# Optimization experiments

Hardware: AMD Instinct MI355X
Metric: run time of the kernel (lower is better)

## Reference

```python
import jax, jax.numpy as jnp
import numpy as np
import math

N_NODES = 50000
N_EDGES = 800000
F_IN = 32
HID = 64


def _layernorm(x, g, b, eps=1e-5):
    mu = x.mean(-1, keepdims=True)
    var = ((x - mu) ** 2).mean(-1, keepdims=True)
    return (x - mu) / jnp.sqrt(var + eps) * g + b


def _tconv(x, src, dst, Wq, bq, Wk, bk, Wv, bv, Ws, heads):
    # PyG TransformerConv (concat=True, root_weight=True, bias=False on skip)
    N = x.shape[0]
    C = Wq.shape[1] // heads
    q = (x @ Wq + bq).reshape(N, heads, C)[dst]  # [E,H,C] gathered at targets
    k = (x @ Wk + bk).reshape(N, heads, C)[src]  # [E,H,C] gathered at sources
    v = (x @ Wv + bv).reshape(N, heads, C)[src]
    scores = (q * k).sum(-1) / math.sqrt(C)      # [E,H]
    m = jax.ops.segment_max(scores, dst, num_segments=N)   # [N,H]
    p = jnp.exp(scores - m[dst])
    denom = jax.ops.segment_sum(p, dst, num_segments=N)
    alpha = p / (denom[dst] + 1e-16)             # segment softmax over in-edges
    agg = jax.ops.segment_sum(v * alpha[..., None], dst, num_segments=N)
    return agg.reshape(N, heads * C) + x @ Ws    # + skip (no bias)


def setup_inputs() -> dict:
    key = jax.random.key(0)
    ks = iter(jax.random.split(key, 64))
    def rn(shape, s=0.1):
        return jax.random.normal(next(ks), shape, jnp.float32) * s
    inp = {
        "x": rn((N_NODES, F_IN), 1.0),
        "edge_index": jax.random.randint(next(ks), (2, N_EDGES), 0, N_NODES, dtype=jnp.int32),
        "ln0_g": jnp.ones((F_IN,), jnp.float32),
        "ln0_b": jnp.zeros((F_IN,), jnp.float32),
    }
    dims = [F_IN, HID, HID]
    for l in range(3):
        d = dims[l]
        inp[f"Wq{l}"] = rn((d, HID)); inp[f"bq{l}"] = rn((HID,), 0.05)
        inp[f"Wk{l}"] = rn((d, HID)); inp[f"bk{l}"] = rn((HID,), 0.05)
        inp[f"Wv{l}"] = rn((d, HID)); inp[f"bv{l}"] = rn((HID,), 0.05)
        inp[f"Ws{l}"] = rn((d, HID))
        inp[f"g{l}"] = jnp.ones((HID,), jnp.float32)
        inp[f"b{l}"] = jnp.zeros((HID,), jnp.float32)
    inp["Wr1"] = rn((HID, HID // 2)); inp["br1"] = jnp.zeros((HID // 2,), jnp.float32)
    inp["Wr2"] = rn((HID // 2, 1));   inp["br2"] = jnp.zeros((1,), jnp.float32)
    inp["Wt1"] = rn((HID, HID // 2)); inp["bt1"] = jnp.zeros((HID // 2,), jnp.float32)
    inp["Wt2"] = rn((HID // 2, 1));   inp["bt2"] = jnp.zeros((1,), jnp.float32)
    return inp


def reference(x, edge_index, ln0_g, ln0_b,
              Wq0, bq0, Wk0, bk0, Wv0, bv0, Ws0, g0, b0,
              Wq1, bq1, Wk1, bk1, Wv1, bv1, Ws1, g1, b1,
              Wq2, bq2, Wk2, bk2, Wv2, bv2, Ws2, g2, b2,
              Wr1, br1, Wr2, br2, Wt1, bt1, Wt2, bt2):
    src, dst = edge_index[0], edge_index[1]
    h = _layernorm(x, ln0_g, ln0_b)
    layers = [
        (Wq0, bq0, Wk0, bk0, Wv0, bv0, Ws0, g0, b0, 4),
        (Wq1, bq1, Wk1, bk1, Wv1, bv1, Ws1, g1, b1, 4),
        (Wq2, bq2, Wk2, bk2, Wv2, bv2, Ws2, g2, b2, 1),
    ]
    for i, (Wq, bq, Wk, bk, Wv, bv, Ws, g, b, heads) in enumerate(layers):
        x_res = h if h.shape[-1] == HID else None
        h = _tconv(h, src, dst, Wq, bq, Wk, bk, Wv, bv, Ws, heads)
        h = _layernorm(h, g, b)
        if x_res is not None and i > 0:
            h = h + 0.1 * x_res
        if i < len(layers) - 1:
            h = jax.nn.relu(h)  # dropout is identity in eval mode
    rtt = jax.nn.relu(h @ Wr1 + br1) @ Wr2 + br2      # [N,1]
    retrans = jax.nn.relu(h @ Wt1 + bt1) @ Wt2 + bt2  # [N,1]
    return jnp.concatenate([rtt, retrans], axis=1)    # [N,2]
```

## Files before the change

### kernel.cpp

```cpp
#include <hip/hip_runtime.h>
#include <hip/hip_bf16.h>
#include <math.h>

#define N_NODES 50000
#define N_EDGES 800000
#define HID 64
#define NBK 196
#define EPB 1024
#define SB  ((N_EDGES + EPB - 1) / EPB)
#define FLAT (NBK * SB)
#define SCAN_B ((FLAT + 255) / 256)

#define LN0_BLKS   6250
#define HIST_BLKS  SB
#define WP0_BLKS   32
#define WP12_BLKS  64
#define PREP_BLKS  (LN0_BLKS + HIST_BLKS + WP0_BLKS + 2 * WP12_BLKS)

typedef __attribute__((ext_vector_type(8))) short short8;
typedef __attribute__((ext_vector_type(4))) float float4v;

__device__ __forceinline__ unsigned short f32_to_bf16_rne(float f) {
    unsigned int u = __float_as_uint(f);
    unsigned int r = u + 0x7fffu + ((u >> 16) & 1u);
    return (unsigned short)(r >> 16);
}

__device__ __forceinline__ void ln0_body(int b, int t,
        const float* __restrict__ x, const float* __restrict__ g,
        const float* __restrict__ bb, float* __restrict__ h0) {
    int lane = t & 63;
    int n = b * 8 + (t >> 6) * 2 + (lane >> 5);
    int c = lane & 31;
    float v = x[n * 32 + c];
    float s = v;
    #pragma unroll
    for (int off = 1; off < 32; off <<= 1) s += __shfl_xor(s, off);
    float mu = s * (1.0f / 32.0f);
    float d = v - mu;
    float vs = d * d;
    #pragma unroll
    for (int off = 1; off < 32; off <<= 1) vs += __shfl_xor(vs, off);
    float var = vs * (1.0f / 32.0f);
    h0[n * 32 + c] = d * rsqrtf(var + 1e-5f) * g[c] + bb[c];
}

__device__ __forceinline__ void wprep_body(int idx, int KS,
        const float* __restrict__ Wq, const float* __restrict__ Wk,
        const float* __restrict__ Wv, const float* __restrict__ Ws,
        unsigned short* __restrict__ Wp) {
    int j = idx & 7;
    int lane = (idx >> 3) & 63;
    int ts = idx >> 9;
    int s = ts % KS;
    int tile = ts / KS;
    int which = tile >> 2;
    int slice = tile & 3;
    int k = s * 32 + ((lane >> 4) * 8) + j;
    int col = slice * 16 + (lane & 15);
    const float* W = (which == 0) ? Wq : (which == 1) ? Wk : (which == 2) ? Wv : Ws;
    Wp[idx] = f32_to_bf16_rne(W[k * 64 + col]);
}

__global__ __launch_bounds__(256) void prep_kernel(
        const float* __restrict__ x, const float* __restrict__ ln0g,
        const float* __restrict__ ln0b, float* __restrict__ h0,
        const int* __restrict__ dst, int* __restrict__ ghist,
        const float* __restrict__ Wq0, const float* __restrict__ Wk0,
        const float* __restrict__ Wv0, const float* __restrict__ Ws0,
        unsigned short* __restrict__ Wp0,
        const float* __restrict__ Wq1, const float* __restrict__ Wk1,
        const float* __restrict__ Wv1, const float* __restrict__ Ws1,
        unsigned short* __restrict__ Wp1,
        const float* __restrict__ Wq2, const float* __restrict__ Wk2,
        const float* __restrict__ Wv2, const float* __restrict__ Ws2,
        unsigned short* __restrict__ Wp2) {
    __shared__ int hist[NBK];
    int b = blockIdx.x;
    int t = threadIdx.x;
    if (b < LN0_BLKS) {
        ln0_body(b, t, x, ln0g, ln0b, h0);
    } else if (b < LN0_BLKS + HIST_BLKS) {
        int i = b - LN0_BLKS;
        for (int k = t; k < NBK; k += 256) hist[k] = 0;
        __syncthreads();
        int e0 = i * EPB;
        #pragma unroll
        for (int r = 0; r < EPB / 256; r++) {
            int e = e0 + r * 256 + t;
            if (e < N_EDGES) atomicAdd(&hist[dst[e] >> 8], 1);
        }
        __syncthreads();
        for (int k = t; k < NBK; k += 256) ghist[k * SB + i] = hist[k];
    } else if (b < LN0_BLKS + HIST_BLKS + WP0_BLKS) {
        int idx = (b - LN0_BLKS - HIST_BLKS) * 256 + t;
        wprep_body(idx, 1, Wq0, Wk0, Wv0, Ws0, Wp0);
    } else if (b < LN0_BLKS + HIST_BLKS + WP0_BLKS + WP12_BLKS) {
        int idx = (b - LN0_BLKS - HIST_BLKS - WP0_BLKS) * 256 + t;
        wprep_body(idx, 2, Wq1, Wk1, Wv1, Ws1, Wp1);
    } else {
        int idx = (b - LN0_BLKS - HIST_BLKS - WP0_BLKS - WP12_BLKS) * 256 + t;
        wprep_body(idx, 2, Wq2, Wk2, Wv2, Ws2, Wp2);
    }
}

__global__ void scan1_kernel(const int* __restrict__ ghist, int* __restrict__ csum) {
    int f = blockIdx.x * 256 + threadIdx.x;
    int v = (f < FLAT) ? ghist[f] : 0;
    #pragma unroll
    for (int off = 1; off < 64; off <<= 1) v += __shfl_xor(v, off);
    __shared__ int ws[4];
    if ((threadIdx.x & 63) == 0) ws[threadIdx.x >> 6] = v;
    __syncthreads();
    if (threadIdx.x == 0) csum[blockIdx.x] = ws[0] + ws[1] + ws[2] + ws[3];
}

__global__ void scan2_kernel(const int* __restrict__ csum, int* __restrict__ coff,
                             int* __restrict__ bbase, int* __restrict__ row_ptr) {
    int lane = threadIdx.x;
    int carry = 0;
    for (int base = 0; base < SCAN_B; base += 64) {
        int i = base + lane;
        int v = (i < SCAN_B) ? csum[i] : 0;
        int incl = v;
        #pragma unroll
        for (int off = 1; off < 64; off <<= 1) {
            int tt = __shfl_up(incl, off);
            if (lane >= off) incl += tt;
        }
        if (i < SCAN_B) coff[i] = carry + incl - v;
        carry += __shfl(incl, 63);
    }
    if (lane == 0) { bbase[NBK] = N_EDGES; row_ptr[N_NODES] = N_EDGES; }
}

__global__ void scan3_kernel(const int* __restrict__ ghist, const int* __restrict__ coff,
                             int* __restrict__ goff, int* __restrict__ bbase) {
    int f = blockIdx.x * 256 + threadIdx.x;
    int lane = threadIdx.x & 63;
    int w = threadIdx.x >> 6;
    int v = (f < FLAT) ? ghist[f] : 0;
    int incl = v;
    #pragma unroll
    for (int off = 1; off < 64; off <<= 1) {
        int tt = __shfl_up(incl, off);
        if (lane >= off) incl += tt;
    }
    __shared__ int ws[4];
    if (lane == 63) ws[w] = incl;
    __syncthreads();
    int woff = 0;
    #pragma unroll
    for (int k = 0; k < 4; k++) if (k < w) woff += ws[k];
    int excl = coff[blockIdx.x] + woff + incl - v;
    if (f < FLAT) {
        goff[f] = excl;
        if (f % SB == 0) bbase[f / SB] = excl;
    }
}

__global__ __launch_bounds__(256) void scatter_kernel(
        const int* __restrict__ src, const int* __restrict__ dst,
        const int* __restrict__ goff, int2* __restrict__ ebkt) {
    __shared__ int hist[NBK];
    int t = threadIdx.x, i = blockIdx.x;
    for (int k = t; k < NBK; k += 256) hist[k] = 0;
    __syncthreads();
    int e0 = i * EPB;
    #pragma unroll
    for (int r = 0; r < EPB / 256; r++) {
        int e = e0 + r * 256 + t;
        if (e < N_EDGES) {
            int s = src[e], d = dst[e];
            int k = d >> 8;
            int rank = atomicAdd(&hist[k], 1);
            ebkt[goff[k * SB + i] + rank] = make_int2(s, d);
        }
    }
}

__global__ __launch_bounds__(256) void bucket_build_kernel(
        const int2* __restrict__ ebkt, const int* __restrict__ bbase,
        int* __restrict__ row_ptr, int* __restrict__ colb) {
    __shared__ int ldeg[256];
    __shared__ int lcur[256];
    __shared__ int wsum[4];
    int b = blockIdx.x;
    int t = threadIdx.x;
    int cbase = bbase[b];
    int cnt = bbase[b + 1] - cbase;

    ldeg[t] = 0;
    __syncthreads();
    for (int i = t; i < cnt; i += 256) {
        int2 e = ebkt[cbase + i];
        atomicAdd(&ldeg[e.y & 255], 1);
    }
    __syncthreads();

    int lane = t & 63;
    int w = t >> 6;
    int v = ldeg[t];
    int incl = v;
    #pragma unroll
    for (int off = 1; off < 64; off <<= 1) {
        int tt = __shfl_up(incl, off);
        if (lane >= off) incl += tt;
    }
    if (lane == 63) wsum[w] = incl;
    __syncthreads();
    int woff = 0;
    #pragma unroll
    for (int k = 0; k < 4; k++) if (k < w) woff += wsum[k];
    int excl = woff + incl - v;

    int node = b * 256 + t;
    if (node < N_NODES) row_ptr[node] = cbase + excl;
    lcur[t] = excl;
    __syncthreads();

    for (int i = t; i < cnt; i += 256) {
        int2 e = ebkt[cbase + i];
        int r = atomicAdd(&lcur[e.y & 255], 1);
        colb[cbase + r] = e.x;
    }
}

template <int D>
__global__ __launch_bounds__(256) void qkvs_mfma_kernel(
        const float* __restrict__ h,
        const unsigned short* __restrict__ Wp,
        const float* __restrict__ bq, const float* __restrict__ bk,
        const float* __restrict__ bv,
        float* __restrict__ Q, unsigned int* __restrict__ KV,
        float* __restrict__ S) {
    constexpr int KS = D / 32;
    int t = threadIdx.x;
    int lane = t & 63;
    int w = t >> 6;
    int n0 = blockIdx.x * 16;
    int n16 = lane & 15;
    int quad = lane >> 4;
    int col = w * 16 + n16;

    short8 afrag[KS];
    #pragma unroll
    for (int s = 0; s < KS; s++) {
        const float* hp = &h[(n0 + n16) * D + s * 32 + quad * 8];
        float4 a0 = *(const float4*)hp;
        float4 a1 = *(const float4*)(hp + 4);
        short8 af;
        af[0] = (short)f32_to_bf16_rne(a0.x);
        af[1] = (short)f32_to_bf16_rne(a0.y);
        af[2] = (short)f32_to_bf16_rne(a0.z);
        af[3] = (short)f32_to_bf16_rne(a0.w);
        af[4] = (short)f32_to_bf16_rne(a1.x);
        af[5] = (short)f32_to_bf16_rne(a1.y);
        af[6] = (short)f32_to_bf16_rne(a1.z);
        af[7] = (short)f32_to_bf16_rne(a1.w);
        afrag[s] = af;
    }

    float4v accs[4];
    #pragma unroll
    for (int which = 0; which < 4; which++) {
        float4v acc = {0.0f, 0.0f, 0.0f, 0.0f};
        int tile = which * 4 + w;
        #pragma unroll
        for (int s = 0; s < KS; s++) {
            short8 bfrag = *(const short8*)&Wp[((tile * KS + s) * 64 + lane) * 8];
            acc = __builtin_amdgcn_mfma_f32_16x16x32_bf16(afrag[s], bfrag, acc, 0, 0, 0);
        }
        accs[which] = acc;
    }

    float bqc = bq[col], bkc = bk[col], bvc = bv[col];

    #pragma unroll
    for (int r = 0; r < 4; r++) {
        int node = n0 + quad * 4 + r;
        Q[node * 64 + col] = accs[0][r] + bqc;
        unsigned int kw = f32_to_bf16_rne(accs[1][r] + bkc);
        unsigned int vw = f32_to_bf16_rne(accs[2][r] + bvc);
        KV[node * 64 + col] = (vw << 16) | kw;
        S[node * 64 + col] = accs[3][r];
    }
}

template <int HEADS, bool RES, bool RELU, bool HEAD>
__global__ __launch_bounds__(256) void agg_kernel(
                           const float* __restrict__ Q, const unsigned int* __restrict__ KV,
                           const float* __restrict__ S,
                           const int* __restrict__ row_ptr, const int* __restrict__ colb,
                           const float* __restrict__ g, const float* __restrict__ b,
                           const float* __restrict__ h_in, float* __restrict__ h_out,
                           const float* __restrict__ Wr1, const float* __restrict__ br1,
                           const float* __restrict__ Wr2, const float* __restrict__ br2,
                           const float* __restrict__ Wt1, const float* __restrict__ bt1,
                           const float* __restrict__ Wt2, const float* __restrict__ bt2,
                           float* __restrict__ out) {
    constexpr int C = HID / HEADS;
    int lane = threadIdx.x & 63;
    int m = lane & 15;
    int grp = lane >> 4;
    int n = blockIdx.x * 4 + (threadIdx.x >> 6);

    const float scale = rsqrtf((float)C);
    float4 q4 = *(const float4*)&Q[n * 64 + 4 * m];
    q4.x *= scale; q4.y *= scale; q4.z *= scale; q4.w *= scale;

    int beg = row_ptr[n], end = row_ptr[n + 1];

    float ssum = 0.0f;
    float acc0 = 0.0f, acc1 = 0.0f, acc2 = 0.0f, acc3 = 0.0f;

    for (int base = beg; base < end; base += 64) {
        int limit = min(end - base, 64);
        int src_l = (base + lane < end) ? colb[base + lane] : 0;
        for (int sub = 0; sub < limit; sub += 16) {
            int e0 = sub + grp, e1 = sub + 4 + grp, e2 = sub + 8 + grp, e3 = sub + 12 + grp;
            int s0 = __shfl(src_l, e0);
            int s1 = __shfl(src_l, e1);
            int s2 = __shfl(src_l, e2);
            int s3 = __shfl(src_l, e3);
            bool v0ok = e0 < limit, v1ok = e1 < limit, v2ok = e2 < limit, v3ok = e3 < limit;
            uint4 kv0 = make_uint4(0, 0, 0, 0), kv1 = kv0, kv2 = kv0, kv3 = kv0;
            if (v0ok) kv0 = *(const uint4*)&KV[(size_t)s0 * 64 + 4 * m];
            if (v1ok) kv1 = *(const uint4*)&KV[(size_t)s1 * 64 + 4 * m];
            if (v2ok) kv2 = *(const uint4*)&KV[(size_t)s2 * 64 + 4 * m];
            if (v3ok) kv3 = *(const uint4*)&KV[(size_t)s3 * 64 + 4 * m];

            float t0 = fmaf(q4.x, __uint_as_float(kv0.x << 16),
                       fmaf(q4.y, __uint_as_float(kv0.y << 16),
                       fmaf(q4.z, __uint_as_float(kv0.z << 16),
                            q4.w * __uint_as_float(kv0.w << 16))));
            float t1 = fmaf(q4.x, __uint_as_float(kv1.x << 16),
                       fmaf(q4.y, __uint_as_float(kv1.y << 16),
                       fmaf(q4.z, __uint_as_float(kv1.z << 16),
                            q4.w * __uint_as_float(kv1.w << 16))));
            float t2 = fmaf(q4.x, __uint_as_float(kv2.x << 16),
                       fmaf(q4.y, __uint_as_float(kv2.y << 16),
                       fmaf(q4.z, __uint_as_float(kv2.z << 16),
                            q4.w * __uint_as_float(kv2.w << 16))));
            float t3 = fmaf(q4.x, __uint_as_float(kv3.x << 16),
                       fmaf(q4.y, __uint_as_float(kv3.y << 16),
                       fmaf(q4.z, __uint_as_float(kv3.z << 16),
                            q4.w * __uint_as_float(kv3.w << 16))));
            #pragma unroll
            for (int off = 1; off < C / 4; off <<= 1) {
                t0 += __shfl_xor(t0, off);
                t1 += __shfl_xor(t1, off);
                t2 += __shfl_xor(t2, off);
                t3 += __shfl_xor(t3, off);
            }
            float p0 = v0ok ? __expf(t0) : 0.0f;
            float p1 = v1ok ? __expf(t1) : 0.0f;
            float p2 = v2ok ? __expf(t2) : 0.0f;
            float p3 = v3ok ? __expf(t3) : 0.0f;
            ssum += (p0 + p1) + (p2 + p3);
            acc0 = fmaf(p0, __uint_as_float(kv0.x & 0xffff0000u),
                   fmaf(p1, __uint_as_float(kv1.x & 0xffff0000u),
                   fmaf(p2, __uint_as_float(kv2.x & 0xffff0000u),
                   fmaf(p3, __uint_as_float(kv3.x & 0xffff0000u), acc0))));
            acc1 = fmaf(p0, __uint_as_float(kv0.y & 0xffff0000u),
                   fmaf(p1, __uint_as_float(kv1.y & 0xffff0000u),
                   fmaf(p2, __uint_as_float(kv2.y & 0xffff0000u),
                   fmaf(p3, __uint_as_float(kv3.y & 0xffff0000u), acc1))));
            acc2 = fmaf(p0, __uint_as_float(kv0.z & 0xffff0000u),
                   fmaf(p1, __uint_as_float(kv1.z & 0xffff0000u),
                   fmaf(p2, __uint_as_float(kv2.z & 0xffff0000u),
                   fmaf(p3, __uint_as_float(kv3.z & 0xffff0000u), acc2))));
            acc3 = fmaf(p0, __uint_as_float(kv0.w & 0xffff0000u),
                   fmaf(p1, __uint_as_float(kv1.w & 0xffff0000u),
                   fmaf(p2, __uint_as_float(kv2.w & 0xffff0000u),
                   fmaf(p3, __uint_as_float(kv3.w & 0xffff0000u), acc3))));
        }
    }

    #pragma unroll
    for (int off = 16; off < 64; off <<= 1) {
        ssum += __shfl_xor(ssum, off);
        acc0 += __shfl_xor(acc0, off);
        acc1 += __shfl_xor(acc1, off);
        acc2 += __shfl_xor(acc2, off);
        acc3 += __shfl_xor(acc3, off);
    }

    float inv = 1.0f / (ssum + 1e-16f);
    float4 sv = *(const float4*)&S[n * 64 + 4 * m];
    float o0 = fmaf(acc0, inv, sv.x);
    float o1 = fmaf(acc1, inv, sv.y);
    float o2 = fmaf(acc2, inv, sv.z);
    float o3 = fmaf(acc3, inv, sv.w);

    float s = (o0 + o1) + (o2 + o3);
    #pragma unroll
    for (int off = 1; off < 16; off <<= 1) s += __shfl_xor(s, off);
    float mu = s * (1.0f / 64.0f);
    float d0 = o0 - mu, d1 = o1 - mu, d2 = o2 - mu, d3 = o3 - mu;
    float vs = (d0 * d0 + d1 * d1) + (d2 * d2 + d3 * d3);
    #pragma unroll
    for (int off = 1; off < 16; off <<= 1) vs += __shfl_xor(vs, off);
    float rstd = rsqrtf(vs * (1.0f / 64.0f) + 1e-5f);

    float4 gv = *(const float4*)&g[4 * m];
    float4 bv = *(const float4*)&b[4 * m];
    float y0 = d0 * rstd * gv.x + bv.x;
    float y1 = d1 * rstd * gv.y + bv.y;
    float y2 = d2 * rstd * gv.z + bv.z;
    float y3 = d3 * rstd * gv.w + bv.w;
    if (RES) {
        float4 rv = *(const float4*)&h_in[n * 64 + 4 * m];
        y0 = fmaf(0.1f, rv.x, y0);
        y1 = fmaf(0.1f, rv.y, y1);
        y2 = fmaf(0.1f, rv.z, y2);
        y3 = fmaf(0.1f, rv.w, y3);
    }
    if (RELU) {
        y0 = fmaxf(y0, 0.0f); y1 = fmaxf(y1, 0.0f);
        y2 = fmaxf(y2, 0.0f); y3 = fmaxf(y3, 0.0f);
    }

    if (!HEAD) {
        if (grp == 0) {
            float4 yv = make_float4(y0, y1, y2, y3);
            *(float4*)&h_out[n * 64 + 4 * m] = yv;
        }
    } else {
        __shared__ float sh[4][HID];
        int wave = threadIdx.x >> 6;
        if (grp == 0) {
            float4 yv = make_float4(y0, y1, y2, y3);
            *(float4*)&sh[wave][4 * m] = yv;
        }
        __syncthreads();
        int half = lane >> 5;
        int j = lane & 31;
        const float* W1 = half ? Wt1 : Wr1;
        const float* b1 = half ? bt1 : br1;
        const float* W2 = half ? Wt2 : Wr2;
        const float* b2v = half ? bt2 : br2;
        float a = b1[j];
        #pragma unroll 8
        for (int i = 0; i < 64; i++) a = fmaf(sh[wave][i], W1[i * 32 + j], a);
        a = fmaxf(a, 0.0f);
        float r = a * W2[j];
        #pragma unroll
        for (int off = 1; off < 32; off <<= 1) r += __shfl_xor(r, off);
        if (j == 0) out[n * 2 + half] = r + b2v[0];
    }
}

extern "C" void kernel_launch(void* const* d_in, const int* in_sizes, int n_in,
                              void* d_out, int out_size, void* d_ws, size_t ws_size,
                              hipStream_t stream) {
    const float* x    = (const float*)d_in[0];
    const int*   ei   = (const int*)d_in[1];
    const int*   src  = ei;
    const int*   dst  = ei + N_EDGES;
    const float* ln0g = (const float*)d_in[2];
    const float* ln0b = (const float*)d_in[3];

    const float* P[27];
    for (int i = 0; i < 27; i++) P[i] = (const float*)d_in[4 + i];
    const float* Wr1 = (const float*)d_in[31];
    const float* br1 = (const float*)d_in[32];
    const float* Wr2 = (const float*)d_in[33];
    const float* br2 = (const float*)d_in[34];
    const float* Wt1 = (const float*)d_in[35];
    const float* bt1 = (const float*)d_in[36];
    const float* Wt2 = (const float*)d_in[37];
    const float* bt2 = (const float*)d_in[38];

    float* out = (float*)d_out;

    float* hbuf0 = (float*)d_ws;
    float* hbuf1 = hbuf0 + N_NODES * 64;
    float* Qb    = hbuf1 + N_NODES * 64;
    float* Sb    = Qb + N_NODES * 64;
    unsigned int* KVb = (unsigned int*)(Sb + N_NODES * 64);
    int* row_ptr = (int*)(KVb + N_NODES * 64);
    int* colb    = row_ptr + (N_NODES + 1);
    int* ghist   = colb + N_EDGES;
    int* goff    = ghist + FLAT;
    int* csum    = goff + FLAT;
    int* coff    = csum + SCAN_B;
    int* bbase   = coff + SCAN_B;
    unsigned short* Wp0 = (unsigned short*)(bbase + NBK + 1);
    unsigned short* Wp1 = Wp0 + 16 * 1 * 512;
    unsigned short* Wp2 = Wp1 + 16 * 2 * 512;
    int2* ebkt = (int2*)Qb;

    prep_kernel<<<PREP_BLKS, 256, 0, stream>>>(x, ln0g, ln0b, hbuf0,
        dst, ghist,
        P[0],  P[2],  P[4],  P[6],  Wp0,
        P[9],  P[11], P[13], P[15], Wp1,
        P[18], P[20], P[22], P[24], Wp2);
    scan1_kernel<<<SCAN_B, 256, 0, stream>>>(ghist, csum);
    scan2_kernel<<<1, 64, 0, stream>>>(csum, coff, bbase, row_ptr);
    scan3_kernel<<<SCAN_B, 256, 0, stream>>>(ghist, coff, goff, bbase);
    scatter_kernel<<<SB, 256, 0, stream>>>(src, dst, goff, ebkt);
    bucket_build_kernel<<<NBK, 256, 0, stream>>>(ebkt, bbase, row_ptr, colb);

    qkvs_mfma_kernel<32><<<3125, 256, 0, stream>>>(hbuf0, Wp0,
        P[1], P[3], P[5], Qb, KVb, Sb);
    agg_kernel<4, false, true, false><<<12500, 256, 0, stream>>>(Qb, KVb, Sb,
        row_ptr, colb, P[7], P[8], nullptr, hbuf1,
        Wr1, br1, Wr2, br2, Wt1, bt1, Wt2, bt2, out);

    qkvs_mfma_kernel<64><<<3125, 256, 0, stream>>>(hbuf1, Wp1,
        P[10], P[12], P[14], Qb, KVb, Sb);
    agg_kernel<4, true, true, false><<<12500, 256, 0, stream>>>(Qb, KVb, Sb,
        row_ptr, colb, P[16], P[17], hbuf1, hbuf0,
        Wr1, br1, Wr2, br2, Wt1, bt1, Wt2, bt2, out);

    qkvs_mfma_kernel<64><<<3125, 256, 0, stream>>>(hbuf0, Wp2,
        P[19], P[21], P[23], Qb, KVb, Sb);
    agg_kernel<1, true, false, true><<<12500, 256, 0, stream>>>(Qb, KVb, Sb,
        row_ptr, colb, P[25], P[26], hbuf0, hbuf1,
        Wr1, br1, Wr2, br2, Wt1, bt1, Wt2, bt2, out);
}
```

Baseline: 337.6 us.

## Pack Q and skip as bf16 pair, fuse layer-0 QKVS into scatter launch

Q (pre-scaled by 1/sqrt(C)) and the skip projection S are now stored as one packed bf16 word per element instead of two fp32 arrays. This halves that traffic and removes the scale multiply from the aggregation kernel. The layer-0 QKVS projection blocks are merged into the edge scatter launch so both run in one grid, and the edge bucket buffer moves to hbuf1. The cost is extra rounding on Q and the skip term, which may shift accuracy.

```diff
diff --git a/kernel.cpp b/kernel.cpp
--- a/kernel.cpp
+++ b/kernel.cpp
@@ -10,6 +10,8 @@
 #define SB  ((N_EDGES + EPB - 1) / EPB)
 #define FLAT (NBK * SB)
 #define SCAN_B ((FLAT + 255) / 256)
+
+#define QKVS0_BLKS 3125
 
 #define LN0_BLKS   6250
 #define HIST_BLKS  SB
@@ -159,86 +161,17 @@
     }
 }
 
-__global__ __launch_bounds__(256) void scatter_kernel(
-        const int* __restrict__ src, const int* __restrict__ dst,
-        const int* __restrict__ goff, int2* __restrict__ ebkt) {
-    __shared__ int hist[NBK];
-    int t = threadIdx.x, i = blockIdx.x;
-    for (int k = t; k < NBK; k += 256) hist[k] = 0;
-    __syncthreads();
-    int e0 = i * EPB;
-    #pragma unroll
-    for (int r = 0; r < EPB / 256; r++) {
-        int e = e0 + r * 256 + t;
-        if (e < N_EDGES) {
-            int s = src[e], d = dst[e];
-            int k = d >> 8;
-            int rank = atomicAdd(&hist[k], 1);
-            ebkt[goff[k * SB + i] + rank] = make_int2(s, d);
-        }
-    }
-}
-
-__global__ __launch_bounds__(256) void bucket_build_kernel(
-        const int2* __restrict__ ebkt, const int* __restrict__ bbase,
-        int* __restrict__ row_ptr, int* __restrict__ colb) {
-    __shared__ int ldeg[256];
-    __shared__ int lcur[256];
-    __shared__ int wsum[4];
-    int b = blockIdx.x;
-    int t = threadIdx.x;
-    int cbase = bbase[b];
-    int cnt = bbase[b + 1] - cbase;
-
-    ldeg[t] = 0;
-    __syncthreads();
-    for (int i = t; i < cnt; i += 256) {
-        int2 e = ebkt[cbase + i];
-        atomicAdd(&ldeg[e.y & 255], 1);
-    }
-    __syncthreads();
-
-    int lane = t & 63;
-    int w = t >> 6;
-    int v = ldeg[t];
-    int incl = v;
-    #pragma unroll
-    for (int off = 1; off < 64; off <<= 1) {
-        int tt = __shfl_up(incl, off);
-        if (lane >= off) incl += tt;
-    }
-    if (lane == 63) wsum[w] = incl;
-    __syncthreads();
-    int woff = 0;
-    #pragma unroll
-    for (int k = 0; k < 4; k++) if (k < w) woff += wsum[k];
-    int excl = woff + incl - v;
-
-    int node = b * 256 + t;
-    if (node < N_NODES) row_ptr[node] = cbase + excl;
-    lcur[t] = excl;
-    __syncthreads();
-
-    for (int i = t; i < cnt; i += 256) {
-        int2 e = ebkt[cbase + i];
-        int r = atomicAdd(&lcur[e.y & 255], 1);
-        colb[cbase + r] = e.x;
-    }
-}
-
 template <int D>
-__global__ __launch_bounds__(256) void qkvs_mfma_kernel(
+__device__ __forceinline__ void qkvs_body(int bid, int t,
         const float* __restrict__ h,
         const unsigned short* __restrict__ Wp,
         const float* __restrict__ bq, const float* __restrict__ bk,
-        const float* __restrict__ bv,
-        float* __restrict__ Q, unsigned int* __restrict__ KV,
-        float* __restrict__ S) {
+        const float* __restrict__ bv, float scale,
+        unsigned int* __restrict__ QS, unsigned int* __restrict__ KV) {
     constexpr int KS = D / 32;
-    int t = threadIdx.x;
     int lane = t & 63;
     int w = t >> 6;
-    int n0 = blockIdx.x * 16;
+    int n0 = bid * 16;
     int n16 = lane & 15;
     int quad = lane >> 4;
     int col = w * 16 + n16;
@@ -279,18 +212,105 @@
     #pragma unroll
     for (int r = 0; r < 4; r++) {
         int node = n0 + quad * 4 + r;
-        Q[node * 64 + col] = accs[0][r] + bqc;
+        unsigned int qw = f32_to_bf16_rne((accs[0][r] + bqc) * scale);
         unsigned int kw = f32_to_bf16_rne(accs[1][r] + bkc);
         unsigned int vw = f32_to_bf16_rne(accs[2][r] + bvc);
+        unsigned int sw = f32_to_bf16_rne(accs[3][r]);
         KV[node * 64 + col] = (vw << 16) | kw;
-        S[node * 64 + col] = accs[3][r];
+        QS[node * 64 + col] = (sw << 16) | qw;
+    }
+}
+
+template <int D>
+__global__ __launch_bounds__(256) void qkvs_mfma_kernel(
+        const float* __restrict__ h,
+        const unsigned short* __restrict__ Wp,
+        const float* __restrict__ bq, const float* __restrict__ bk,
+        const float* __restrict__ bv, float scale,
+        unsigned int* __restrict__ QS, unsigned int* __restrict__ KV) {
+    qkvs_body<D>(blockIdx.x, threadIdx.x, h, Wp, bq, bk, bv, scale, QS, KV);
+}
+
+__global__ __launch_bounds__(256) void scatter_qkvs0_kernel(
+        const int* __restrict__ src, const int* __restrict__ dst,
+        const int* __restrict__ goff, int2* __restrict__ ebkt,
+        const float* __restrict__ h, const unsigned short* __restrict__ Wp,
+        const float* __restrict__ bq, const float* __restrict__ bk,
+        const float* __restrict__ bv, float scale,
+        unsigned int* __restrict__ QS, unsigned int* __restrict__ KV) {
+    __shared__ int hist[NBK];
+    int t = threadIdx.x;
+    if (blockIdx.x < SB) {
+        int i = blockIdx.x;
+        for (int k = t; k < NBK; k += 256) hist[k] = 0;
+        __syncthreads();
+        int e0 = i * EPB;
+        #pragma unroll
+        for (int r = 0; r < EPB / 256; r++) {
+            int e = e0 + r * 256 + t;
+            if (e < N_EDGES) {
+                int s = src[e], d = dst[e];
+                int k = d >> 8;
+                int rank = atomicAdd(&hist[k], 1);
+                ebkt[goff[k * SB + i] + rank] = make_int2(s, d);
+            }
+        }
+    } else {
+        qkvs_body<32>(blockIdx.x - SB, t, h, Wp, bq, bk, bv, scale, QS, KV);
+    }
+}
+
+__global__ __launch_bounds__(256) void bucket_build_kernel(
+        const int2* __restrict__ ebkt, const int* __restrict__ bbase,
+        int* __restrict__ row_ptr, int* __restrict__ colb) {
+    __shared__ int ldeg[256];
+    __shared__ int lcur[256];
+    __shared__ int wsum[4];
+    int b = blockIdx.x;
+    int t = threadIdx.x;
+    int cbase = bbase[b];
+    int cnt = bbase[b + 1] - cbase;
+
+    ldeg[t] = 0;
+    __syncthreads();
+    for (int i = t; i < cnt; i += 256) {
+        int2 e = ebkt[cbase + i];
+        atomicAdd(&ldeg[e.y & 255], 1);
+    }
+    __syncthreads();
+
+    int lane = t & 63;
+    int w = t >> 6;
+    int v = ldeg[t];
+    int incl = v;
+    #pragma unroll
+    for (int off = 1; off < 64; off <<= 1) {
+        int tt = __shfl_up(incl, off);
+        if (lane >= off) incl += tt;
+    }
+    if (lane == 63) wsum[w] = incl;
+    __syncthreads();
+    int woff = 0;
+    #pragma unroll
+    for (int k = 0; k < 4; k++) if (k < w) woff += wsum[k];
+    int excl = woff + incl - v;
+
+    int node = b * 256 + t;
+    if (node < N_NODES) row_ptr[node] = cbase + excl;
+    lcur[t] = excl;
+    __syncthreads();
+
+    for (int i = t; i < cnt; i += 256) {
+        int2 e = ebkt[cbase + i];
+        int r = atomicAdd(&lcur[e.y & 255], 1);
+        colb[cbase + r] = e.x;
     }
 }
 
 template <int HEADS, bool RES, bool RELU, bool HEAD>
 __global__ __launch_bounds__(256) void agg_kernel(
-                           const float* __restrict__ Q, const unsigned int* __restrict__ KV,
-                           const float* __restrict__ S,
+                           const unsigned int* __restrict__ QS,
+                           const unsigned int* __restrict__ KV,
                            const int* __restrict__ row_ptr, const int* __restrict__ colb,
                            const float* __restrict__ g, const float* __restrict__ b,
                            const float* __restrict__ h_in, float* __restrict__ h_out,
@@ -305,9 +325,11 @@
     int grp = lane >> 4;
     int n = blockIdx.x * 4 + (threadIdx.x >> 6);
 
-    const float scale = rsqrtf((float)C);
-    float4 q4 = *(const float4*)&Q[n * 64 + 4 * m];
-    q4.x *= scale; q4.y *= scale; q4.z *= scale; q4.w *= scale;
+    uint4 qs = *(const uint4*)&QS[n * 64 + 4 * m];
+    float4 q4 = make_float4(__uint_as_float(qs.x << 16),
+                            __uint_as_float(qs.y << 16),
+                            __uint_as_float(qs.z << 16),
+                            __uint_as_float(qs.w << 16));
 
     int beg = row_ptr[n], end = row_ptr[n + 1];
 
@@ -387,11 +409,10 @@
     }
 
     float inv = 1.0f / (ssum + 1e-16f);
-    float4 sv = *(const float4*)&S[n * 64 + 4 * m];
-    float o0 = fmaf(acc0, inv, sv.x);
-    float o1 = fmaf(acc1, inv, sv.y);
-    float o2 = fmaf(acc2, inv, sv.z);
-    float o3 = fmaf(acc3, inv, sv.w);
+    float o0 = fmaf(acc0, inv, __uint_as_float(qs.x & 0xffff0000u));
+    float o1 = fmaf(acc1, inv, __uint_as_float(qs.y & 0xffff0000u));
+    float o2 = fmaf(acc2, inv, __uint_as_float(qs.z & 0xffff0000u));
+    float o3 = fmaf(acc3, inv, __uint_as_float(qs.w & 0xffff0000u));
 
     float s = (o0 + o1) + (o2 + o3);
     #pragma unroll
@@ -476,9 +497,8 @@
 
     float* hbuf0 = (float*)d_ws;
     float* hbuf1 = hbuf0 + N_NODES * 64;
-    float* Qb    = hbuf1 + N_NODES * 64;
-    float* Sb    = Qb + N_NODES * 64;
-    unsigned int* KVb = (unsigned int*)(Sb + N_NODES * 64);
+    unsigned int* QSb = (unsigned int*)(hbuf1 + N_NODES * 64);
+    unsigned int* KVb = QSb + N_NODES * 64;
     int* row_ptr = (int*)(KVb + N_NODES * 64);
     int* colb    = row_ptr + (N_NODES + 1);
     int* ghist   = colb + N_EDGES;
@@ -489,7 +509,7 @@
     unsigned short* Wp0 = (unsigned short*)(bbase + NBK + 1);
     unsigned short* Wp1 = Wp0 + 16 * 1 * 512;
     unsigned short* Wp2 = Wp1 + 16 * 2 * 512;
-    int2* ebkt = (int2*)Qb;
+    int2* ebkt = (int2*)hbuf1;
 
     prep_kernel<<<PREP_BLKS, 256, 0, stream>>>(x, ln0g, ln0b, hbuf0,
         dst, ghist,
@@ -499,24 +519,23 @@
     scan1_kernel<<<SCAN_B, 256, 0, stream>>>(ghist, csum);
     scan2_kernel<<<1, 64, 0, stream>>>(csum, coff, bbase, row_ptr);
     scan3_kernel<<<SCAN_B, 256, 0, stream>>>(ghist, coff, goff, bbase);
-    scatter_kernel<<<SB, 256, 0, stream>>>(src, dst, goff, ebkt);
+    scatter_qkvs0_kernel<<<SB + QKVS0_BLKS, 256, 0, stream>>>(src, dst, goff, ebkt,
+        hbuf0, Wp0, P[1], P[3], P[5], 0.25f, QSb, KVb);
     bucket_build_kernel<<<NBK, 256, 0, stream>>>(ebkt, bbase, row_ptr, colb);
 
-    qkvs_mfma_kernel<32><<<3125, 256, 0, stream>>>(hbuf0, Wp0,
-        P[1], P[3], P[5], Qb, KVb, Sb);
-    agg_kernel<4, false, true, false><<<12500, 256, 0, stream>>>(Qb, KVb, Sb,
+    agg_kernel<4, false, true, false><<<12500, 256, 0, stream>>>(QSb, KVb,
         row_ptr, colb, P[7], P[8], nullptr, hbuf1,
         Wr1, br1, Wr2, br2, Wt1, bt1, Wt2, bt2, out);
 
     qkvs_mfma_kernel<64><<<3125, 256, 0, stream>>>(hbuf1, Wp1,
-        P[10], P[12], P[14], Qb, KVb, Sb);
-    agg_kernel<4, true, true, false><<<12500, 256, 0, stream>>>(Qb, KVb, Sb,
+        P[10], P[12], P[14], 0.25f, QSb, KVb);
+    agg_kernel<4, true, true, false><<<12500, 256, 0, stream>>>(QSb, KVb,
         row_ptr, colb, P[16], P[17], hbuf1, hbuf0,
         Wr1, br1, Wr2, br2, Wt1, bt1, Wt2, bt2, out);
 
     qkvs_mfma_kernel<64><<<3125, 256, 0, stream>>>(hbuf0, Wp2,
-        P[19], P[21], P[23], Qb, KVb, Sb);
-    agg_kernel<1, true, false, true><<<12500, 256, 0, stream>>>(Qb, KVb, Sb,
+        P[19], P[21], P[23], 0.125f, QSb, KVb);
+    agg_kernel<1, true, false, true><<<12500, 256, 0, stream>>>(QSb, KVb,
         row_ptr, colb, P[25], P[26], hbuf0, hbuf1,
         Wr1, br1, Wr2, br2, Wt1, bt1, Wt2, bt2, out);
 }
```

Result: faster. 324.4 us (-3.9%).
